# Kernel optimization log

Measured on AMD Instinct MI355X. Metric: run time of the kernel, lower is better.

The kernel has to match this reference:

```python
import jax, jax.numpy as jnp
import numpy as np

CE_WEIGHT = 1.0
TRIPLET_WEIGHT = 0.1
MARGIN = 0.2


def setup_inputs() -> dict:
    key = jax.random.key(0)
    k1, k2, k3 = jax.random.split(key, 3)
    B, D, V = 4096, 512, 6000
    logits = jax.random.normal(k1, (B, V), dtype=jnp.float32)
    embeddings = jax.random.normal(k2, (B, D), dtype=jnp.float32)
    labels = jax.random.randint(k3, (B,), 0, 512, dtype=jnp.int64)
    return {"logits": logits, "embeddings": embeddings, "labels": labels}


def _pairwise_dist(emb):
    # Euclidean cdist via gram matrix; safe sqrt (zero grad where d2 == 0).
    sq = jnp.sum(emb * emb, axis=-1)  # [B]
    d2 = sq[:, None] + sq[None, :] - 2.0 * (emb @ emb.T)  # [B, B]
    d2 = jnp.maximum(d2, 0.0)
    safe = jnp.where(d2 > 0.0, d2, 1.0)
    return jnp.where(d2 > 0.0, jnp.sqrt(safe), 0.0)


def _losses(logits, embeddings, labels):
    B = logits.shape[0]
    # Cross entropy (mean reduction, matching nn.CrossEntropyLoss).
    logp = jax.nn.log_softmax(logits, axis=-1)
    ce_loss = -jnp.mean(jnp.take_along_axis(logp, labels[:, None], axis=1)[:, 0])

    # Batch-hard triplet loss, fully vectorized (one masked amax/amin per row).
    dist = _pairwise_dist(embeddings)  # [B, B]
    same = labels[:, None] == labels[None, :]  # [B, B]
    eye = jnp.eye(B, dtype=bool)
    pos_mask = same & ~eye
    neg_mask = ~same
    neg_inf = jnp.float32(-np.inf)
    pos_inf = jnp.float32(np.inf)
    hardest_pos = jnp.max(jnp.where(pos_mask, dist, neg_inf), axis=1)  # [B]
    hardest_neg = jnp.min(jnp.where(neg_mask, dist, pos_inf), axis=1)  # [B]
    valid = jnp.any(pos_mask, axis=1) & jnp.any(neg_mask, axis=1)  # [B]
    per_row = jax.nn.relu(hardest_pos - hardest_neg + MARGIN)
    per_row = jnp.where(valid, per_row, 0.0)
    n_valid = jnp.sum(valid.astype(jnp.float32))
    triplet_loss = jnp.where(n_valid > 0, jnp.sum(per_row) / jnp.maximum(n_valid, 1.0), 0.0)

    total_loss = CE_WEIGHT * ce_loss + TRIPLET_WEIGHT * triplet_loss
    return total_loss, ce_loss, triplet_loss


def reference(logits, embeddings, labels):
    return _losses(logits, embeddings, labels)
```

## Files before the change

kernel.cpp:

```cpp
#include <hip/hip_runtime.h>
#include <hip/hip_bf16.h>
#include <math.h>

#define BN   4096
#define DN   512
#define VN   6000
#define NCLS 512

typedef __attribute__((ext_vector_type(8)))  short short8;
typedef __attribute__((ext_vector_type(16))) float f32x16;

__device__ __forceinline__ unsigned short f2bf(float x) {
  unsigned int u = __float_as_uint(x);
  u = (u + 0x7FFFu + ((u >> 16) & 1u)) >> 16;
  return (unsigned short)u;
}

__device__ __forceinline__ void gld_lds16(const unsigned short* g, unsigned short* l) {
  __builtin_amdgcn_global_load_lds(
      (const __attribute__((address_space(1))) void*)g,
      (__attribute__((address_space(3))) void*)l, 16, 0, 0);
}

__launch_bounds__(256)
__global__ void prep_kernel(const float* __restrict__ emb, const int* __restrict__ labels,
                            unsigned short* __restrict__ embh, float* __restrict__ sqn,
                            int* __restrict__ cnt, int* __restrict__ posb,
                            int* __restrict__ negb) {
  const int row  = blockIdx.x * 4 + (threadIdx.x >> 6);
  const int lane = threadIdx.x & 63;
  const float4* rp = (const float4*)(emb + (size_t)row * DN);
  float4 a = rp[lane];
  float4 b = rp[lane + 64];
  float ss = a.x * a.x + a.y * a.y + a.z * a.z + a.w * a.w
           + b.x * b.x + b.y * b.y + b.z * b.z + b.w * b.w;
  ushort4 ha, hb;
  ha.x = f2bf(a.x); ha.y = f2bf(a.y); ha.z = f2bf(a.z); ha.w = f2bf(a.w);
  hb.x = f2bf(b.x); hb.y = f2bf(b.y); hb.z = f2bf(b.z); hb.w = f2bf(b.w);
  ushort4* wp = (ushort4*)(embh + (size_t)row * DN);
  wp[lane] = ha;
  wp[lane + 64] = hb;
#pragma unroll
  for (int off = 1; off < 64; off <<= 1) ss += __shfl_xor(ss, off);
  if (lane == 0) {
    sqn[row] = ss;
    posb[row] = 0;
    negb[row] = 0x7F800000;
    atomicAdd(cnt + labels[row], 1);
  }
}

__device__ __forceinline__ void triplet_job(int t, unsigned short* sA, unsigned short* sB,
                                            const unsigned short* __restrict__ embh,
                                            const float* __restrict__ sqn,
                                            const int* __restrict__ labels,
                                            int* __restrict__ posb,
                                            int* __restrict__ negb, int lane) {
  const int m = lane & 31;
  const int half = lane >> 5;

  int J = (int)((sqrtf(8.f * (float)t + 1.f) - 1.f) * 0.5f);
  while ((J + 1) * (J + 2) / 2 <= t) ++J;
  while (J * (J + 1) / 2 > t) --J;
  const int I = t - J * (J + 1) / 2;
  const int i0 = I * 64, j0 = J * 64;
  const bool diag = (I == J);

  const int lrow = lane >> 3;
  const int lchk = (lane & 7) ^ lrow;
  const unsigned short* gA = embh + (size_t)(i0 + lrow) * DN + lchk * 8;
  const unsigned short* gB = embh + (size_t)(j0 + lrow) * DN + lchk * 8;

  f32x16 acc[2][2] = {};
  f32x16 accT[2][2] = {};

  for (int ks = 0; ks < 8; ++ks) {
    const int kk = ks * 64;
    asm volatile("s_waitcnt lgkmcnt(0)" ::: "memory");
#pragma unroll
    for (int s = 0; s < 8; ++s)
      gld_lds16(gA + kk + (size_t)s * 8 * DN, &sA[s * 8 * 64]);
#pragma unroll
    for (int s = 0; s < 8; ++s)
      gld_lds16(gB + kk + (size_t)s * 8 * DN, &sB[s * 8 * 64]);
    asm volatile("s_waitcnt vmcnt(0)" ::: "memory");
#pragma unroll
    for (int q = 0; q < 4; ++q) {
      const int c = q * 2 + half;
      const int sw = ((c ^ (m & 7)) * 8);
      short8 a0 = *(const short8*)&sA[m * 64 + sw];
      short8 a1 = *(const short8*)&sA[(32 + m) * 64 + sw];
      short8 b0 = *(const short8*)&sB[m * 64 + sw];
      short8 b1 = *(const short8*)&sB[(32 + m) * 64 + sw];
      acc[0][0]  = __builtin_amdgcn_mfma_f32_32x32x16_bf16(a0, b0, acc[0][0], 0, 0, 0);
      acc[0][1]  = __builtin_amdgcn_mfma_f32_32x32x16_bf16(a0, b1, acc[0][1], 0, 0, 0);
      acc[1][0]  = __builtin_amdgcn_mfma_f32_32x32x16_bf16(a1, b0, acc[1][0], 0, 0, 0);
      acc[1][1]  = __builtin_amdgcn_mfma_f32_32x32x16_bf16(a1, b1, acc[1][1], 0, 0, 0);
      accT[0][0] = __builtin_amdgcn_mfma_f32_32x32x16_bf16(b0, a0, accT[0][0], 0, 0, 0);
      accT[0][1] = __builtin_amdgcn_mfma_f32_32x32x16_bf16(b0, a1, accT[0][1], 0, 0, 0);
      accT[1][0] = __builtin_amdgcn_mfma_f32_32x32x16_bf16(b1, a0, accT[1][0], 0, 0, 0);
      accT[1][1] = __builtin_amdgcn_mfma_f32_32x32x16_bf16(b1, a1, accT[1][1], 0, 0, 0);
    }
  }

  {
    const int gj0 = j0 + m, gj1 = j0 + 32 + m;
    const int cl0 = labels[gj0], cl1 = labels[gj1];
    const float cq0 = sqn[gj0], cq1 = sqn[gj1];
    float p0 = 0.f, p1 = 0.f, n0 = INFINITY, n1 = INFINITY;
#pragma unroll
    for (int rb = 0; rb < 2; ++rb) {
#pragma unroll
      for (int r = 0; r < 16; ++r) {
        const int gi = i0 + rb * 32 + (r & 3) + 8 * (r >> 2) + 4 * half;
        const int rl = labels[gi];
        const float rq = sqn[gi];
        const float d0 = fmaf(-2.f, acc[rb][0][r], rq + cq0);
        const float d1 = fmaf(-2.f, acc[rb][1][r], rq + cq1);
        if (rl == cl0) { if (gi != gj0) p0 = fmaxf(p0, d0); } else n0 = fminf(n0, d0);
        if (rl == cl1) { if (gi != gj1) p1 = fmaxf(p1, d1); } else n1 = fminf(n1, d1);
      }
    }
    p0 = fmaxf(p0, __shfl_xor(p0, 32)); n0 = fminf(n0, __shfl_xor(n0, 32));
    p1 = fmaxf(p1, __shfl_xor(p1, 32)); n1 = fminf(n1, __shfl_xor(n1, 32));
    if (half == 0) {
      atomicMax(posb + gj0, __float_as_int(p0));
      atomicMin(negb + gj0, __float_as_int(n0));
      atomicMax(posb + gj1, __float_as_int(p1));
      atomicMin(negb + gj1, __float_as_int(n1));
    }
  }

  if (!diag) {
    const int gj0 = i0 + m, gj1 = i0 + 32 + m;
    const int cl0 = labels[gj0], cl1 = labels[gj1];
    const float cq0 = sqn[gj0], cq1 = sqn[gj1];
    float p0 = 0.f, p1 = 0.f, n0 = INFINITY, n1 = INFINITY;
#pragma unroll
    for (int rb = 0; rb < 2; ++rb) {
#pragma unroll
      for (int r = 0; r < 16; ++r) {
        const int gi = j0 + rb * 32 + (r & 3) + 8 * (r >> 2) + 4 * half;
        const int rl = labels[gi];
        const float rq = sqn[gi];
        const float d0 = fmaf(-2.f, accT[rb][0][r], rq + cq0);
        const float d1 = fmaf(-2.f, accT[rb][1][r], rq + cq1);
        if (rl == cl0) p0 = fmaxf(p0, d0); else n0 = fminf(n0, d0);
        if (rl == cl1) p1 = fmaxf(p1, d1); else n1 = fminf(n1, d1);
      }
    }
    p0 = fmaxf(p0, __shfl_xor(p0, 32)); n0 = fminf(n0, __shfl_xor(n0, 32));
    p1 = fmaxf(p1, __shfl_xor(p1, 32)); n1 = fminf(n1, __shfl_xor(n1, 32));
    if (half == 0) {
      atomicMax(posb + gj0, __float_as_int(p0));
      atomicMin(negb + gj0, __float_as_int(n0));
      atomicMax(posb + gj1, __float_as_int(p1));
      atomicMin(negb + gj1, __float_as_int(n1));
    }
  }
}

__launch_bounds__(64, 2)
__global__ void fused_kernel(const float* __restrict__ logits,
                             const int* __restrict__ labels,
                             float* __restrict__ ce_part,
                             const unsigned short* __restrict__ embh,
                             const float* __restrict__ sqn,
                             int* __restrict__ posb, int* __restrict__ negb) {
  __shared__ unsigned short smem[8192];
  const int b = blockIdx.x;
  const int lane = threadIdx.x;

  int trip_job, ce_row;
  if (b < 32) {
    trip_job = 2048 + b; ce_row = -1;
  } else {
    const int g = (b - 32) / 3, r = (b - 32) % 3;
    if (r == 0) { trip_job = g; ce_row = -1; }
    else        { trip_job = -1; ce_row = g * 2 + (r - 1); }
  }

  if (trip_job >= 0) {
    triplet_job(trip_job, smem, smem + 4096, embh, sqn, labels, posb, negb, lane);
    return;
  }

  const float* rp = logits + (size_t)ce_row * VN;
  const float xlab = rp[labels[ce_row]];
  const float4* q = (const float4*)rp;
  float4 v[24];
#pragma unroll
  for (int u = 0; u < 23; ++u) v[u] = q[lane + u * 64];
  if (lane < 28) v[23] = q[lane + 23 * 64];
  float s = 0.f;
#pragma unroll
  for (int u = 0; u < 23; ++u)
    s += __expf(v[u].x) + __expf(v[u].y) + __expf(v[u].z) + __expf(v[u].w);
  if (lane < 28)
    s += __expf(v[23].x) + __expf(v[23].y) + __expf(v[23].z) + __expf(v[23].w);
#pragma unroll
  for (int off = 1; off < 64; off <<= 1) s += __shfl_xor(s, off);
  if (lane == 0) ce_part[ce_row] = logf(s) - xlab;
}

__launch_bounds__(1024)
__global__ void finalize_kernel(const int* __restrict__ posb, const int* __restrict__ negb,
                                const int* __restrict__ labels, const int* __restrict__ cnt,
                                const float* __restrict__ ce_part, float* __restrict__ out) {
  const int tid = threadIdx.x;
  float cesum = 0.f, sum = 0.f, nv = 0.f;
#pragma unroll
  for (int u = 0; u < 4; ++u) {
    const int i = tid + u * 1024;
    cesum += ce_part[i];
    int c = cnt[labels[i]];
    float p = sqrtf(fmaxf(__int_as_float(posb[i]), 0.f));
    float n = sqrtf(fmaxf(__int_as_float(negb[i]), 0.f));
    float t = fmaxf(p - n + 0.2f, 0.f);
    if (c >= 2 && c < BN) { sum += t; nv += 1.f; }
  }
#pragma unroll
  for (int off = 1; off < 64; off <<= 1) {
    cesum += __shfl_xor(cesum, off);
    sum   += __shfl_xor(sum, off);
    nv    += __shfl_xor(nv, off);
  }
  __shared__ float s0[16], s1[16], s2[16];
  if ((tid & 63) == 0) { s0[tid >> 6] = cesum; s1[tid >> 6] = sum; s2[tid >> 6] = nv; }
  __syncthreads();
  if (tid == 0) {
    cesum = 0.f; sum = 0.f; nv = 0.f;
#pragma unroll
    for (int wv = 0; wv < 16; ++wv) { cesum += s0[wv]; sum += s1[wv]; nv += s2[wv]; }
    float trip = (nv > 0.f) ? sum / nv : 0.f;
    float ce = cesum * (1.f / BN);
    out[0] = ce + 0.1f * trip;
    out[1] = ce;
    out[2] = trip;
  }
}

extern "C" void kernel_launch(void* const* d_in, const int* in_sizes, int n_in,
                              void* d_out, int out_size, void* d_ws, size_t ws_size,
                              hipStream_t stream) {
  const float* logits = (const float*)d_in[0];
  const float* emb    = (const float*)d_in[1];
  const int*   labels = (const int*)d_in[2];
  float* out = (float*)d_out;

  char* ws = (char*)d_ws;
  unsigned short* embh = (unsigned short*)ws;
  float* sqn    = (float*)(ws + (size_t)BN * DN * 2);
  int*   posb   = (int*)((char*)sqn  + (size_t)BN * 4);
  int*   negb   = (int*)((char*)posb + (size_t)BN * 4);
  int*   cnt    = (int*)((char*)negb + (size_t)BN * 4);
  float* ce_part = (float*)((char*)cnt + (size_t)NCLS * 4);

  hipMemsetAsync(cnt, 0, (size_t)NCLS * 4, stream);
  hipLaunchKernelGGL(prep_kernel, dim3(BN / 4), dim3(256), 0, stream,
                     emb, labels, embh, sqn, cnt, posb, negb);
  hipLaunchKernelGGL(fused_kernel, dim3(32 + 2048 * 3), dim3(64), 0, stream,
                     logits, labels, ce_part, embh, sqn, posb, negb);
  hipLaunchKernelGGL(finalize_kernel, dim3(1), dim3(1024), 0, stream,
                     posb, negb, labels, cnt, ce_part, out);
}
```

Measured before the change: 182.0 us.

## Use 128x128 four-wave triplet tiles with double-buffered LDS staging

Triplet Gram tiles grow from 64x64 single-wave blocks to 128x128 blocks with four waves, so each loaded embedding row is reused across twice as many outputs. Global-to-LDS loads are double-buffered so the next k-slice streams in while MFMAs run on the current one. Labels and squared norms are staged in shared memory for the epilogue, and CE blocks now handle four rows each. The cost is larger LDS use (64KB per block) and extra barriers, which may reduce occupancy.

```diff
diff --git a/kernel.cpp b/kernel.cpp
--- a/kernel.cpp
+++ b/kernel.cpp
@@ -50,48 +50,77 @@
   }
 }
 
-__device__ __forceinline__ void triplet_job(int t, unsigned short* sA, unsigned short* sB,
-                                            const unsigned short* __restrict__ embh,
-                                            const float* __restrict__ sqn,
-                                            const int* __restrict__ labels,
-                                            int* __restrict__ posb,
-                                            int* __restrict__ negb, int lane) {
-  const int m = lane & 31;
+__device__ __forceinline__ void trip128(int t, unsigned short* smem,
+                                        const unsigned short* __restrict__ embh,
+                                        const float* __restrict__ sqn,
+                                        const int* __restrict__ labels,
+                                        int* __restrict__ posb,
+                                        int* __restrict__ negb, int tid) {
+  const int lane = tid & 63;
+  const int w    = tid >> 6;
+  const int wi   = w >> 1;
+  const int wj   = w & 1;
+  const int m    = lane & 31;
   const int half = lane >> 5;
 
   int J = (int)((sqrtf(8.f * (float)t + 1.f) - 1.f) * 0.5f);
   while ((J + 1) * (J + 2) / 2 <= t) ++J;
   while (J * (J + 1) / 2 > t) --J;
   const int I = t - J * (J + 1) / 2;
-  const int i0 = I * 64, j0 = J * 64;
-  const bool diag = (I == J);
+  const int i0 = I * 128, j0 = J * 128;
+  const bool qdiag = (I == J) && (wi == wj);
+
+  const int   side = tid >> 7;
+  const int   idx  = tid & 127;
+  const int   grow = (side ? j0 : i0) + idx;
+  const int   lme  = labels[grow];
+  const float qme  = sqn[grow];
 
   const int lrow = lane >> 3;
   const int lchk = (lane & 7) ^ lrow;
-  const unsigned short* gA = embh + (size_t)(i0 + lrow) * DN + lchk * 8;
-  const unsigned short* gB = embh + (size_t)(j0 + lrow) * DN + lchk * 8;
+  const int prow = w * 8 + lrow;
+  const unsigned short* gA = embh + (size_t)(i0 + prow) * DN + lchk * 8;
+  const unsigned short* gB = embh + (size_t)(j0 + prow) * DN + lchk * 8;
+
+#define TJ_STAGE(bufoff, kk)                                                  \
+  do {                                                                        \
+    _Pragma("unroll")                                                         \
+    for (int s = 0; s < 4; ++s)                                               \
+      gld_lds16(gA + (kk) + (size_t)s * 32 * DN,                              \
+                smem + (bufoff) + (s * 32 + w * 8) * 64);                     \
+    _Pragma("unroll")                                                         \
+    for (int s = 0; s < 4; ++s)                                               \
+      gld_lds16(gB + (kk) + (size_t)s * 32 * DN,                              \
+                smem + (bufoff) + 8192 + (s * 32 + w * 8) * 64);              \
+  } while (0)
 
   f32x16 acc[2][2] = {};
   f32x16 accT[2][2] = {};
 
+  TJ_STAGE(0, 0);
+
+#pragma unroll
   for (int ks = 0; ks < 8; ++ks) {
-    const int kk = ks * 64;
+    const int cur = (ks & 1) * 16384;
     asm volatile("s_waitcnt lgkmcnt(0)" ::: "memory");
-#pragma unroll
-    for (int s = 0; s < 8; ++s)
-      gld_lds16(gA + kk + (size_t)s * 8 * DN, &sA[s * 8 * 64]);
-#pragma unroll
-    for (int s = 0; s < 8; ++s)
-      gld_lds16(gB + kk + (size_t)s * 8 * DN, &sB[s * 8 * 64]);
-    asm volatile("s_waitcnt vmcnt(0)" ::: "memory");
+    __builtin_amdgcn_s_barrier();
+    if (ks < 7) {
+      TJ_STAGE(16384 - cur, (ks + 1) * 64);
+      asm volatile("s_waitcnt vmcnt(8)" ::: "memory");
+    } else {
+      asm volatile("s_waitcnt vmcnt(0)" ::: "memory");
+    }
+    __builtin_amdgcn_s_barrier();
+    const unsigned short* sA = smem + cur;
+    const unsigned short* sB = smem + cur + 8192;
 #pragma unroll
     for (int q = 0; q < 4; ++q) {
       const int c = q * 2 + half;
-      const int sw = ((c ^ (m & 7)) * 8);
-      short8 a0 = *(const short8*)&sA[m * 64 + sw];
-      short8 a1 = *(const short8*)&sA[(32 + m) * 64 + sw];
-      short8 b0 = *(const short8*)&sB[m * 64 + sw];
-      short8 b1 = *(const short8*)&sB[(32 + m) * 64 + sw];
+      const int sw = (c ^ (m & 7)) * 8;
+      short8 a0 = *(const short8*)&sA[(wi * 64 + m) * 64 + sw];
+      short8 a1 = *(const short8*)&sA[(wi * 64 + 32 + m) * 64 + sw];
+      short8 b0 = *(const short8*)&sB[(wj * 64 + m) * 64 + sw];
+      short8 b1 = *(const short8*)&sB[(wj * 64 + 32 + m) * 64 + sw];
       acc[0][0]  = __builtin_amdgcn_mfma_f32_32x32x16_bf16(a0, b0, acc[0][0], 0, 0, 0);
       acc[0][1]  = __builtin_amdgcn_mfma_f32_32x32x16_bf16(a0, b1, acc[0][1], 0, 0, 0);
       acc[1][0]  = __builtin_amdgcn_mfma_f32_32x32x16_bf16(a1, b0, acc[1][0], 0, 0, 0);
@@ -102,19 +131,28 @@
       accT[1][1] = __builtin_amdgcn_mfma_f32_32x32x16_bf16(b1, a1, accT[1][1], 0, 0, 0);
     }
   }
+#undef TJ_STAGE
+
+  int*   sLab = (int*)smem;
+  float* sQn  = (float*)(smem + 512);
+  sLab[tid] = lme;
+  sQn[tid]  = qme;
+  __syncthreads();
 
   {
-    const int gj0 = j0 + m, gj1 = j0 + 32 + m;
-    const int cl0 = labels[gj0], cl1 = labels[gj1];
-    const float cq0 = sqn[gj0], cq1 = sqn[gj1];
+    const int jb  = 128 + wj * 64;
+    const int gj0 = j0 + wj * 64 + m, gj1 = gj0 + 32;
+    const int cl0 = sLab[jb + m], cl1 = sLab[jb + 32 + m];
+    const float cq0 = sQn[jb + m], cq1 = sQn[jb + 32 + m];
     float p0 = 0.f, p1 = 0.f, n0 = INFINITY, n1 = INFINITY;
 #pragma unroll
     for (int rb = 0; rb < 2; ++rb) {
 #pragma unroll
       for (int r = 0; r < 16; ++r) {
-        const int gi = i0 + rb * 32 + (r & 3) + 8 * (r >> 2) + 4 * half;
-        const int rl = labels[gi];
-        const float rq = sqn[gi];
+        const int ri = wi * 64 + rb * 32 + (r & 3) + 8 * (r >> 2) + 4 * half;
+        const int gi = i0 + ri;
+        const int rl = sLab[ri];
+        const float rq = sQn[ri];
         const float d0 = fmaf(-2.f, acc[rb][0][r], rq + cq0);
         const float d1 = fmaf(-2.f, acc[rb][1][r], rq + cq1);
         if (rl == cl0) { if (gi != gj0) p0 = fmaxf(p0, d0); } else n0 = fminf(n0, d0);
@@ -131,18 +169,18 @@
     }
   }
 
-  if (!diag) {
-    const int gj0 = i0 + m, gj1 = i0 + 32 + m;
-    const int cl0 = labels[gj0], cl1 = labels[gj1];
-    const float cq0 = sqn[gj0], cq1 = sqn[gj1];
+  if (!qdiag) {
+    const int gj0 = i0 + wi * 64 + m, gj1 = gj0 + 32;
+    const int cl0 = sLab[wi * 64 + m], cl1 = sLab[wi * 64 + 32 + m];
+    const float cq0 = sQn[wi * 64 + m], cq1 = sQn[wi * 64 + 32 + m];
     float p0 = 0.f, p1 = 0.f, n0 = INFINITY, n1 = INFINITY;
 #pragma unroll
     for (int rb = 0; rb < 2; ++rb) {
 #pragma unroll
       for (int r = 0; r < 16; ++r) {
-        const int gi = j0 + rb * 32 + (r & 3) + 8 * (r >> 2) + 4 * half;
-        const int rl = labels[gi];
-        const float rq = sqn[gi];
+        const int rj = wj * 64 + rb * 32 + (r & 3) + 8 * (r >> 2) + 4 * half;
+        const int rl = sLab[128 + rj];
+        const float rq = sQn[128 + rj];
         const float d0 = fmaf(-2.f, accT[rb][0][r], rq + cq0);
         const float d1 = fmaf(-2.f, accT[rb][1][r], rq + cq1);
         if (rl == cl0) p0 = fmaxf(p0, d0); else n0 = fminf(n0, d0);
@@ -160,31 +198,33 @@
   }
 }
 
-__launch_bounds__(64, 2)
+__launch_bounds__(256, 2)
 __global__ void fused_kernel(const float* __restrict__ logits,
                              const int* __restrict__ labels,
                              float* __restrict__ ce_part,
                              const unsigned short* __restrict__ embh,
                              const float* __restrict__ sqn,
                              int* __restrict__ posb, int* __restrict__ negb) {
-  __shared__ unsigned short smem[8192];
+  __shared__ unsigned short smem[32768];
   const int b = blockIdx.x;
-  const int lane = threadIdx.x;
-
-  int trip_job, ce_row;
-  if (b < 32) {
-    trip_job = 2048 + b; ce_row = -1;
+  const int tid = threadIdx.x;
+
+  int trip_job, ce_base;
+  if (b < 16) {
+    trip_job = 512 + b; ce_base = -1;
   } else {
-    const int g = (b - 32) / 3, r = (b - 32) % 3;
-    if (r == 0) { trip_job = g; ce_row = -1; }
-    else        { trip_job = -1; ce_row = g * 2 + (r - 1); }
+    const int g = (b - 16) / 3, r = (b - 16) % 3;
+    if (r == 0) { trip_job = g; ce_base = -1; }
+    else        { trip_job = -1; ce_base = (g * 2 + (r - 1)) * 4; }
   }
 
   if (trip_job >= 0) {
-    triplet_job(trip_job, smem, smem + 4096, embh, sqn, labels, posb, negb, lane);
+    trip128(trip_job, smem, embh, sqn, labels, posb, negb, tid);
     return;
   }
 
+  const int ce_row = ce_base + (tid >> 6);
+  const int lane = tid & 63;
   const float* rp = logits + (size_t)ce_row * VN;
   const float xlab = rp[labels[ce_row]];
   const float4* q = (const float4*)rp;
@@ -259,7 +299,7 @@
   hipMemsetAsync(cnt, 0, (size_t)NCLS * 4, stream);
   hipLaunchKernelGGL(prep_kernel, dim3(BN / 4), dim3(256), 0, stream,
                      emb, labels, embh, sqn, cnt, posb, negb);
-  hipLaunchKernelGGL(fused_kernel, dim3(32 + 2048 * 3), dim3(64), 0, stream,
+  hipLaunchKernelGGL(fused_kernel, dim3(16 + 512 * 3), dim3(256), 0, stream,
                      logits, labels, ce_part, embh, sqn, posb, negb);
   hipLaunchKernelGGL(finalize_kernel, dim3(1), dim3(1024), 0, stream,
                      posb, negb, labels, cnt, ce_part, out);
```

Result: faster. 171.6 us (-5.7%).
